# Optimization experiments

Hardware: AMD Instinct MI355X
Metric: run time of the kernel (lower is better)

The kernel has to match this reference:

```python
import jax, jax.numpy as jnp
import numpy as np

N, D, E, TOP_K = 2048, 512, 16, 2
HID = 4 * D
EPS = 1e-10


def setup_inputs() -> dict:
    key = jax.random.key(0)
    ks = jax.random.split(key, 8)
    s = 0.02
    return {
        "x": jax.random.normal(ks[0], (N, D), dtype=jnp.float32),
        "w_norm": jnp.ones((D,), dtype=jnp.float32),
        "Wr": jax.random.normal(ks[1], (D, E), dtype=jnp.float32) * s,
        "br": jnp.zeros((E,), dtype=jnp.float32),
        "W1": jax.random.normal(ks[2], (E, D, HID), dtype=jnp.float32) * s,
        "b1": jnp.zeros((E, HID), dtype=jnp.float32),
        "W2": jax.random.normal(ks[3], (E, HID, D), dtype=jnp.float32) * s,
        "b2": jnp.zeros((E, D), dtype=jnp.float32),
    }


def reference(x, w_norm, Wr, br, W1, b1, W2, b2):
    res = x
    # RMSNorm over feature dim (dim=1 in the torch code for 2D input)
    rms = jnp.sqrt(jnp.mean(x * x, axis=1, keepdims=True) + EPS)
    xn = w_norm * (x / rms)
    # Router: top-k over expert logits, softmax over the k selected logits
    logits = xn @ Wr + br                      # [N, E]
    top_p, top_i = jax.lax.top_k(logits, TOP_K)  # [N, k]
    top_p = jax.nn.softmax(top_p, axis=-1)
    # Dense per-token expert weights [N, E] (top-k indices are distinct)
    weight = jnp.zeros((x.shape[0], E), dtype=x.dtype)
    weight = weight.at[jnp.arange(x.shape[0])[:, None], top_i].add(top_p)
    # All-expert FFN (dense reference for the routed dispatch)
    h = jnp.einsum("nd,edh->enh", xn, W1) + b1[:, None, :]   # [E, N, 4D]
    y = jnp.einsum("enh,ehd->end", jax.nn.silu(h), W2) + b2[:, None, :]  # [E, N, D]
    out = jnp.einsum("end,ne->nd", y, weight)
    return out + res
```

## Files before the change

kernel.cpp:

```cpp
#include <hip/hip_runtime.h>

#define N_TOK 2048
#define DIM   512
#define NEXP  16
#define HID   2048
#define NSLOT (N_TOK*2)

typedef __attribute__((ext_vector_type(8))) short short8;
typedef __attribute__((ext_vector_type(4))) float floatx4;

__device__ __forceinline__ ushort f2bf(float f) {
    union { float f; unsigned u; } c; c.f = f;
    unsigned u = c.u;
    unsigned r = (u + 0x7fffu + ((u >> 16) & 1u)) >> 16;
    return (ushort)r;
}
__device__ __forceinline__ float bf2f(ushort u) {
    union { unsigned u; float f; } c; c.u = ((unsigned)u) << 16;
    return c.f;
}

__device__ __forceinline__ void gl_lds16(const void* g, void* l) {
    __builtin_amdgcn_global_load_lds(
        (const __attribute__((address_space(1))) unsigned int*)g,
        (__attribute__((address_space(3))) unsigned int*)l, 16, 0, 0);
}

__device__ __forceinline__ void transpose_tile(const float* __restrict__ src,
                                               ushort* __restrict__ dst,
                                               int K, int Nn, int bx, void* smem)
{
    float* Ls = (float*)smem;
    const int NT = Nn >> 6;
    const int KT = K >> 6;
    const int nt = bx % NT; bx /= NT;
    const int kt = bx % KT; bx /= KT;
    const int e  = bx;
    const int t = threadIdx.x;

    const float* sp = src + ((size_t)e * K + kt * 64) * Nn + nt * 64;
#pragma unroll
    for (int i = 0; i < 4; i++) {
        const int k  = (t >> 4) + i * 16;
        const int c4 = (t & 15) * 4;
        const float4 v = *(const float4*)(sp + (size_t)k * Nn + c4);
        Ls[k * 65 + c4 + 0] = v.x;
        Ls[k * 65 + c4 + 1] = v.y;
        Ls[k * 65 + c4 + 2] = v.z;
        Ls[k * 65 + c4 + 3] = v.w;
    }
    __syncthreads();

    ushort* dp = dst + ((size_t)e * Nn + nt * 64) * K + kt * 64;
#pragma unroll
    for (int i = 0; i < 2; i++) {
        const int n = (t >> 3) + i * 32;
        const int c = t & 7;
        unsigned w[4];
#pragma unroll
        for (int q = 0; q < 4; q++) {
            const unsigned lo = f2bf(Ls[(c * 8 + q * 2 + 0) * 65 + n]);
            const unsigned hi = f2bf(Ls[(c * 8 + q * 2 + 1) * 65 + n]);
            w[q] = lo | (hi << 16);
        }
        uint4 o = make_uint4(w[0], w[1], w[2], w[3]);
        *(uint4*)(dp + (size_t)n * K + c * 8) = o;
    }
}

__global__ __launch_bounds__(256)
void router_fused(const float* __restrict__ x, const float* __restrict__ w_norm,
                  const float* __restrict__ Wr, const float* __restrict__ br,
                  ushort* __restrict__ xn, int2* __restrict__ rec_e,
                  float2* __restrict__ rec_w)
{
    __shared__ float xs[16][516];
    __shared__ float wrT[16][516];

    const int tid  = threadIdx.x;
    const int wave = tid >> 6, lane = tid & 63;
    const int tblk = blockIdx.x * 16;

#pragma unroll
    for (int k = 0; k < 32; k++) {
        const int idx = tid + k * 256;
        wrT[idx & 15][idx >> 4] = Wr[idx];
    }

    const float4* wnp = (const float4*)w_norm;
    const float4 wa = wnp[lane], wb = wnp[lane + 64];
#pragma unroll
    for (int i = 0; i < 4; i++) {
        const int tl = wave * 4 + i, t = tblk + tl;
        const float4* xp = (const float4*)(x + (size_t)t * DIM);
        const float4 a = xp[lane], b = xp[lane + 64];
        float ss = a.x*a.x + a.y*a.y + a.z*a.z + a.w*a.w
                 + b.x*b.x + b.y*b.y + b.z*b.z + b.w*b.w;
#pragma unroll
        for (int m = 32; m >= 1; m >>= 1) ss += __shfl_xor(ss, m, 64);
        const float rinv = 1.f / sqrtf(ss * (1.f / (float)DIM) + 1e-10f);
        float4 na, nb;
        na.x = a.x * wa.x * rinv; na.y = a.y * wa.y * rinv;
        na.z = a.z * wa.z * rinv; na.w = a.w * wa.w * rinv;
        nb.x = b.x * wb.x * rinv; nb.y = b.y * wb.y * rinv;
        nb.z = b.z * wb.z * rinv; nb.w = b.w * wb.w * rinv;
        *(float4*)&xs[tl][lane * 4]       = na;
        *(float4*)&xs[tl][256 + lane * 4] = nb;
        ushort4 ua, ub;
        ua.x = f2bf(na.x); ua.y = f2bf(na.y); ua.z = f2bf(na.z); ua.w = f2bf(na.w);
        ub.x = f2bf(nb.x); ub.y = f2bf(nb.y); ub.z = f2bf(nb.z); ub.w = f2bf(nb.w);
        ushort4* xo = (ushort4*)(xn + (size_t)t * DIM);
        xo[lane] = ua; xo[lane + 64] = ub;
    }
    __syncthreads();

    const int tl = tid >> 4, e = tid & 15;
    const int t = tblk + tl;
    float acc = 0.f;
#pragma unroll 4
    for (int d = 0; d < DIM; d += 4) {
        const float4 xv = *(const float4*)&xs[tl][d];
        const float4 wv = *(const float4*)&wrT[e][d];
        acc += xv.x * wv.x + xv.y * wv.y + xv.z * wv.z + xv.w * wv.w;
    }
    const float v = acc + br[e];

    float m0 = v; int i0 = e; float m1 = -1e30f; int i1 = 16;
#pragma unroll
    for (int msk = 1; msk < 16; msk <<= 1) {
        const float om0 = __shfl_xor(m0, msk, 64); const int oi0 = __shfl_xor(i0, msk, 64);
        const float om1 = __shfl_xor(m1, msk, 64); const int oi1 = __shfl_xor(i1, msk, 64);
        const bool bf_ = (om0 > m0) || (om0 == m0 && oi0 < i0);
        const float t0m = bf_ ? om0 : m0; const int t0i = bf_ ? oi0 : i0;
        const float l0m = bf_ ? m0 : om0; const int l0i = bf_ ? i0 : oi0;
        const bool b2_ = (om1 > m1) || (om1 == m1 && oi1 < i1);
        const float t2m = b2_ ? om1 : m1; const int t2i = b2_ ? oi1 : i1;
        const bool lw = (l0m > t2m) || (l0m == t2m && l0i < t2i);
        m0 = t0m; i0 = t0i;
        m1 = lw ? l0m : t2m; i1 = lw ? l0i : t2i;
    }
    if (e == 0) {
        const float ex = expf(m1 - m0);
        const float w0 = 1.f / (1.f + ex);
        rec_e[t] = make_int2(i0, i1);
        rec_w[t] = make_float2(w0, ex * w0);
    }
}

__global__ __launch_bounds__(256)
void plan_trw1_kernel(const int2* __restrict__ rec_e, int* __restrict__ cnt,
                      int* __restrict__ off, int* __restrict__ tok_of_slot,
                      int* __restrict__ rec_slot,
                      const float* __restrict__ w1src, ushort* __restrict__ w1dst)
{
    __shared__ __align__(16) char smem[16640];

    if (blockIdx.x != 0) {
        transpose_tile(w1src, w1dst, DIM, HID, blockIdx.x - 1, smem);
        return;
    }

    int* soff = (int*)smem;
    const int tid = threadIdx.x;
    const int wv = tid >> 6, lane = tid & 63;

#pragma unroll
    for (int s = 0; s < 4; s++) {
        const int e = wv * 4 + s;
        int total = 0;
        for (int c = 0; c < N_TOK / 64; c++) {
            const int2 er = rec_e[c * 64 + lane];
            const bool hit = (er.x == e) || (er.y == e);
            total += __popcll(__ballot(hit));
        }
        if (lane == 0) soff[e + 1] = total;
    }
    __syncthreads();
    if (tid == 0) {
        soff[0] = 0;
        for (int q = 1; q <= 16; q++) soff[q] += soff[q - 1];
    }
    __syncthreads();

#pragma unroll
    for (int s = 0; s < 4; s++) {
        const int e = wv * 4 + s;
        int base = soff[e];
        if (lane == 0) { cnt[e] = soff[e + 1] - base; off[e] = base; }
        for (int c = 0; c < N_TOK / 64; c++) {
            const int t = c * 64 + lane;
            const int2 er = rec_e[t];
            const bool hit = (er.x == e) || (er.y == e);
            const unsigned long long b = __ballot(hit);
            if (hit) {
                const int slot = base + __popcll(b & ((1ull << lane) - 1ull));
                tok_of_slot[slot] = t;
                const int which = (er.y == e) ? 1 : 0;
                rec_slot[t * 2 + which] = slot;
            }
            base += __popcll(b);
        }
    }
}

template<int MODE>
__device__ __forceinline__ void gemm_body(const ushort* __restrict__ A, int a_stride,
                 const ushort* __restrict__ WT, int wt_k,
                 const float* __restrict__ bias,
                 const int* __restrict__ cnt, const int* __restrict__ off,
                 const int* __restrict__ tok_of_slot,
                 ushort* __restrict__ hout, ushort* __restrict__ yout,
                 int flat, void* smem)
{
    const int x = flat & 7;
    const int g = flat >> 3;
    int e, mt, nb, z;
    if (MODE == 0) {
        e  = x + ((g >> 7) << 3);
        const int r = g & 127;
        nb = r & 31; mt = r >> 5; z = 0;
    } else {
        const int G = ((g >> 5) << 3) + x;
        e = G >> 2; z = G & 3;
        const int idx = g & 31;
        mt = idx >> 3; nb = idx & 7;
    }

    const int count = cnt[e];
    if (mt * 128 >= count) return;
    const int base = off[e];
    const int rows = min(128, count - mt * 128);
    const int n0   = nb * 64;
    const int Nn   = (MODE == 0) ? HID : DIM;
    const int kbeg = (MODE == 0) ? 0 : (z * 512);
    ushort* yp = (MODE == 0) ? nullptr : (yout + (size_t)z * NSLOT * DIM);

    ushort* As_ = (ushort*)smem;
    ushort* Bs_ = (ushort*)((char*)smem + 16384);
    int*    toks = (int*)((char*)smem + 24576);

    const int tid = threadIdx.x;
    if (tid < 128) {
        const int r = tid < rows ? tid : rows - 1;
        const int slot = base + mt * 128 + r;
        toks[tid] = (MODE == 0) ? tok_of_slot[slot] : slot;
    }
    __syncthreads();

    const int lane = tid & 63;
    const int wid  = tid >> 6;
    const int wm = wid >> 1, wn = wid & 1;
    const int fr = lane & 15, fg = lane >> 4;

    const int rl  = lane >> 2;
    const int sko = ((lane & 3) ^ ((lane >> 4) & 3)) * 8;

    const ushort* aptr[2];
    const ushort* wbase = WT + (size_t)e * Nn * wt_k + (size_t)n0 * wt_k;
#pragma unroll
    for (int j = 0; j < 2; j++) {
        const int s = wid * 2 + j;
        aptr[j] = A + (size_t)toks[s * 16 + rl] * a_stride + sko;
    }
    const ushort* bptr = wbase + (size_t)(wid * 16 + rl) * wt_k + sko;

    floatx4 acc[4][2];
#pragma unroll
    for (int mi = 0; mi < 4; mi++)
#pragma unroll
        for (int ni = 0; ni < 2; ni++)
#pragma unroll
            for (int r = 0; r < 4; r++) acc[mi][ni][r] = 0.f;

#define STAGE(pb, k0)                                                              \
    do {                                                                           \
        _Pragma("unroll")                                                          \
        for (int j = 0; j < 2; j++)                                                \
            gl_lds16(aptr[j] + (k0), (void*)(&As_[(pb) * 4096 + (wid * 2 + j) * 512])); \
        gl_lds16(bptr + (k0), (void*)(&Bs_[(pb) * 2048 + wid * 512]));             \
    } while (0)

    int cur = 0;
    STAGE(0, kbeg);

    const int cxor = (fr >> 2) & 3;
    for (int kt = 0; kt < 16; kt++) {
        if (kt < 15) {
            STAGE(cur ^ 1, kbeg + (kt + 1) * 32);
            asm volatile("s_waitcnt vmcnt(3)" ::: "memory");
        } else {
            asm volatile("s_waitcnt vmcnt(0)" ::: "memory");
        }
        __builtin_amdgcn_s_barrier();
        __builtin_amdgcn_sched_barrier(0);

        __builtin_amdgcn_s_setprio(1);
        {
            const int co = (fg ^ cxor) * 8;
            short8 af[4], bfr[2];
#pragma unroll
            for (int mi = 0; mi < 4; mi++)
                af[mi] = *(const short8*)&As_[cur * 4096 + (wm * 64 + mi * 16 + fr) * 32 + co];
#pragma unroll
            for (int ni = 0; ni < 2; ni++)
                bfr[ni] = *(const short8*)&Bs_[cur * 2048 + (wn * 32 + ni * 16 + fr) * 32 + co];
#pragma unroll
            for (int mi = 0; mi < 4; mi++)
#pragma unroll
                for (int ni = 0; ni < 2; ni++)
                    acc[mi][ni] = __builtin_amdgcn_mfma_f32_16x16x32_bf16(af[mi], bfr[ni], acc[mi][ni], 0, 0, 0);
        }
        __builtin_amdgcn_s_setprio(0);

        __builtin_amdgcn_sched_barrier(0);
        __builtin_amdgcn_s_barrier();
        cur ^= 1;
    }
#undef STAGE

#pragma unroll
    for (int ni = 0; ni < 2; ni++) {
        const int gn = n0 + wn * 32 + ni * 16 + fr;
        const float bv = (MODE == 0) ? bias[e * HID + gn] : 0.f;
#pragma unroll
        for (int mi = 0; mi < 4; mi++) {
#pragma unroll
            for (int r = 0; r < 4; r++) {
                const int lm = wm * 64 + mi * 16 + fg * 4 + r;
                if (lm < rows) {
                    const int slot = base + mt * 128 + lm;
                    float v = acc[mi][ni][r];
                    if (MODE == 0) {
                        v += bv;
                        v = v / (1.f + __expf(-v));
                        hout[(size_t)slot * HID + gn] = f2bf(v);
                    } else {
                        yp[(size_t)slot * DIM + gn] = f2bf(v);
                    }
                }
            }
        }
    }
}

__global__ __launch_bounds__(256)
void gemm1_trw2_kernel(const ushort* __restrict__ A,
                       const ushort* __restrict__ W1T,
                       const float* __restrict__ b1,
                       const int* __restrict__ cnt, const int* __restrict__ off,
                       const int* __restrict__ tok_of_slot,
                       ushort* __restrict__ hout,
                       const float* __restrict__ w2src, ushort* __restrict__ w2dst)
{
    __shared__ __align__(16) char smem[25088];
    if (blockIdx.y >= 64) {
        const int bx = (blockIdx.y - 64) * 32 + blockIdx.x;
        transpose_tile(w2src, w2dst, HID, DIM, bx, smem);
        return;
    }
    const int flat = blockIdx.x + (blockIdx.y << 5);
    gemm_body<0>(A, DIM, W1T, DIM, b1, cnt, off, tok_of_slot, hout, nullptr,
                 flat, smem);
}

__global__ __launch_bounds__(256)
void gemm2_kernel(const ushort* __restrict__ A,
                  const ushort* __restrict__ W2T,
                  const int* __restrict__ cnt, const int* __restrict__ off,
                  ushort* __restrict__ yout)
{
    __shared__ __align__(16) char smem[25088];
    const int flat = blockIdx.x + (blockIdx.y << 5);
    gemm_body<1>(A, HID, W2T, HID, nullptr, cnt, off, nullptr, nullptr, yout,
                 flat, smem);
}

__global__ __launch_bounds__(128)
void gather_kernel(const float* __restrict__ x, const ushort* __restrict__ ypart,
                   const float* __restrict__ b2,
                   const int2* __restrict__ rec_e, const float2* __restrict__ rec_w,
                   const int2* __restrict__ rec_slot, float* __restrict__ out)
{
    const int t = blockIdx.x;
    const int d4 = threadIdx.x * 4;
    const int2 ei = rec_e[t];
    const float2 w = rec_w[t];
    const int2 sl = rec_slot[t];
    const float4 xv  = *(const float4*)(x  + (size_t)t * DIM + d4);
    float4 s0 = make_float4(0.f, 0.f, 0.f, 0.f);
    float4 s1 = make_float4(0.f, 0.f, 0.f, 0.f);
#pragma unroll
    for (int kc = 0; kc < 4; kc++) {
        const ushort* yp = ypart + (size_t)kc * NSLOT * DIM;
        const ushort4 a = *(const ushort4*)(yp + (size_t)sl.x * DIM + d4);
        const ushort4 b = *(const ushort4*)(yp + (size_t)sl.y * DIM + d4);
        s0.x += bf2f(a.x); s0.y += bf2f(a.y); s0.z += bf2f(a.z); s0.w += bf2f(a.w);
        s1.x += bf2f(b.x); s1.y += bf2f(b.y); s1.z += bf2f(b.z); s1.w += bf2f(b.w);
    }
    const float4 b0  = *(const float4*)(b2 + (size_t)ei.x * DIM + d4);
    const float4 b1v = *(const float4*)(b2 + (size_t)ei.y * DIM + d4);
    float4 o;
    o.x = xv.x + w.x * (s0.x + b0.x) + w.y * (s1.x + b1v.x);
    o.y = xv.y + w.x * (s0.y + b0.y) + w.y * (s1.y + b1v.y);
    o.z = xv.z + w.x * (s0.z + b0.z) + w.y * (s1.z + b1v.z);
    o.w = xv.w + w.x * (s0.w + b0.w) + w.y * (s1.w + b1v.w);
    *(float4*)(out + (size_t)t * DIM + d4) = o;
}

extern "C" void kernel_launch(void* const* d_in, const int* in_sizes, int n_in,
                              void* d_out, int out_size, void* d_ws, size_t ws_size,
                              hipStream_t stream)
{
    const float* x  = (const float*)d_in[0];
    const float* wn = (const float*)d_in[1];
    const float* Wr = (const float*)d_in[2];
    const float* br = (const float*)d_in[3];
    const float* W1 = (const float*)d_in[4];
    const float* b1 = (const float*)d_in[5];
    const float* W2 = (const float*)d_in[6];
    const float* b2 = (const float*)d_in[7];
    float* out = (float*)d_out;

    char* ws = (char*)d_ws;
    ushort* W1T   = (ushort*)(ws);
    ushort* W2T   = (ushort*)(ws + (32u << 20));
    ushort* xn    = (ushort*)(ws + (64u << 20));
    ushort* h_buf = (ushort*)(ws + (66u << 20));
    ushort* y_par = (ushort*)(ws + (82u << 20));
    char* p = ws + (114u << 20);
    int*    cnt         = (int*)p;    p += 256;
    int*    off         = (int*)p;    p += 256;
    int2*   rec_e       = (int2*)p;   p += N_TOK * 8;
    float2* rec_w       = (float2*)p; p += N_TOK * 8;
    int2*   rec_slot    = (int2*)p;   p += N_TOK * 8;
    int*    tok_of_slot = (int*)p;    p += NSLOT * 4;

    router_fused<<<N_TOK / 16, 256, 0, stream>>>(x, wn, Wr, br, xn, rec_e, rec_w);

    plan_trw1_kernel<<<1 + NEXP * 8 * 32, 256, 0, stream>>>(
        rec_e, cnt, off, tok_of_slot, (int*)rec_slot, W1, W1T);

    gemm1_trw2_kernel<<<dim3(32, 192), 256, 0, stream>>>(
        xn, W1T, b1, cnt, off, tok_of_slot, h_buf, W2, W2T);

    gemm2_kernel<<<dim3(32, 64), 256, 0, stream>>>(h_buf, W2T, cnt, off, y_par);

    gather_kernel<<<N_TOK, 128, 0, stream>>>(x, y_par, b2, rec_e, rec_w, rec_slot, out);
}
```

Before: 116.2 us.

## Remove split-K from second expert GEMM and write fp32 output directly

```diff
diff --git a/kernel.cpp b/kernel.cpp
--- a/kernel.cpp
+++ b/kernel.cpp
@@ -209,21 +209,20 @@
                  const float* __restrict__ bias,
                  const int* __restrict__ cnt, const int* __restrict__ off,
                  const int* __restrict__ tok_of_slot,
-                 ushort* __restrict__ hout, ushort* __restrict__ yout,
+                 ushort* __restrict__ hout, float* __restrict__ yout,
                  int flat, void* smem)
 {
     const int x = flat & 7;
     const int g = flat >> 3;
-    int e, mt, nb, z;
+    int e, mt, nb;
     if (MODE == 0) {
         e  = x + ((g >> 7) << 3);
         const int r = g & 127;
-        nb = r & 31; mt = r >> 5; z = 0;
+        nb = r & 31; mt = r >> 5;
     } else {
-        const int G = ((g >> 5) << 3) + x;
-        e = G >> 2; z = G & 3;
-        const int idx = g & 31;
-        mt = idx >> 3; nb = idx & 7;
+        e  = x + ((g >> 5) << 3);
+        const int r = g & 31;
+        nb = r & 7; mt = r >> 3;
     }
 
     const int count = cnt[e];
@@ -232,8 +231,7 @@
     const int rows = min(128, count - mt * 128);
     const int n0   = nb * 64;
     const int Nn   = (MODE == 0) ? HID : DIM;
-    const int kbeg = (MODE == 0) ? 0 : (z * 512);
-    ushort* yp = (MODE == 0) ? nullptr : (yout + (size_t)z * NSLOT * DIM);
+    const int NKT  = (MODE == 0) ? 16 : 64;
 
     ushort* As_ = (ushort*)smem;
     ushort* Bs_ = (ushort*)((char*)smem + 16384);
@@ -281,12 +279,12 @@
     } while (0)
 
     int cur = 0;
-    STAGE(0, kbeg);
+    STAGE(0, 0);
 
     const int cxor = (fr >> 2) & 3;
-    for (int kt = 0; kt < 16; kt++) {
-        if (kt < 15) {
-            STAGE(cur ^ 1, kbeg + (kt + 1) * 32);
+    for (int kt = 0; kt < NKT; kt++) {
+        if (kt < NKT - 1) {
+            STAGE(cur ^ 1, (kt + 1) * 32);
             asm volatile("s_waitcnt vmcnt(3)" ::: "memory");
         } else {
             asm volatile("s_waitcnt vmcnt(0)" ::: "memory");
@@ -335,7 +333,7 @@
                         v = v / (1.f + __expf(-v));
                         hout[(size_t)slot * HID + gn] = f2bf(v);
                     } else {
-                        yp[(size_t)slot * DIM + gn] = f2bf(v);
+                        yout[(size_t)slot * DIM + gn] = v;
                     }
                 }
             }
@@ -367,7 +365,7 @@
 void gemm2_kernel(const ushort* __restrict__ A,
                   const ushort* __restrict__ W2T,
                   const int* __restrict__ cnt, const int* __restrict__ off,
-                  ushort* __restrict__ yout)
+                  float* __restrict__ yout)
 {
     __shared__ __align__(16) char smem[25088];
     const int flat = blockIdx.x + (blockIdx.y << 5);
@@ -376,7 +374,7 @@
 }
 
 __global__ __launch_bounds__(128)
-void gather_kernel(const float* __restrict__ x, const ushort* __restrict__ ypart,
+void gather_kernel(const float* __restrict__ x, const float* __restrict__ y,
                    const float* __restrict__ b2,
                    const int2* __restrict__ rec_e, const float2* __restrict__ rec_w,
                    const int2* __restrict__ rec_slot, float* __restrict__ out)
@@ -386,17 +384,9 @@
     const int2 ei = rec_e[t];
     const float2 w = rec_w[t];
     const int2 sl = rec_slot[t];
-    const float4 xv  = *(const float4*)(x  + (size_t)t * DIM + d4);
-    float4 s0 = make_float4(0.f, 0.f, 0.f, 0.f);
-    float4 s1 = make_float4(0.f, 0.f, 0.f, 0.f);
-#pragma unroll
-    for (int kc = 0; kc < 4; kc++) {
-        const ushort* yp = ypart + (size_t)kc * NSLOT * DIM;
-        const ushort4 a = *(const ushort4*)(yp + (size_t)sl.x * DIM + d4);
-        const ushort4 b = *(const ushort4*)(yp + (size_t)sl.y * DIM + d4);
-        s0.x += bf2f(a.x); s0.y += bf2f(a.y); s0.z += bf2f(a.z); s0.w += bf2f(a.w);
-        s1.x += bf2f(b.x); s1.y += bf2f(b.y); s1.z += bf2f(b.z); s1.w += bf2f(b.w);
-    }
+    const float4 xv = *(const float4*)(x + (size_t)t * DIM + d4);
+    const float4 s0 = *(const float4*)(y + (size_t)sl.x * DIM + d4);
+    const float4 s1 = *(const float4*)(y + (size_t)sl.y * DIM + d4);
     const float4 b0  = *(const float4*)(b2 + (size_t)ei.x * DIM + d4);
     const float4 b1v = *(const float4*)(b2 + (size_t)ei.y * DIM + d4);
     float4 o;
@@ -426,7 +416,7 @@
     ushort* W2T   = (ushort*)(ws + (32u << 20));
     ushort* xn    = (ushort*)(ws + (64u << 20));
     ushort* h_buf = (ushort*)(ws + (66u << 20));
-    ushort* y_par = (ushort*)(ws + (82u << 20));
+    float*  y_buf = (float*) (ws + (82u << 20));
     char* p = ws + (114u << 20);
     int*    cnt         = (int*)p;    p += 256;
     int*    off         = (int*)p;    p += 256;
@@ -443,7 +433,7 @@
     gemm1_trw2_kernel<<<dim3(32, 192), 256, 0, stream>>>(
         xn, W1T, b1, cnt, off, tok_of_slot, h_buf, W2, W2T);
 
-    gemm2_kernel<<<dim3(32, 64), 256, 0, stream>>>(h_buf, W2T, cnt, off, y_par);
-
-    gather_kernel<<<N_TOK, 128, 0, stream>>>(x, y_par, b2, rec_e, rec_w, rec_slot, out);
-}
+    gemm2_kernel<<<dim3(32, 16), 256, 0, stream>>>(h_buf, W2T, cnt, off, y_buf);
+
+    gather_kernel<<<N_TOK, 128, 0, stream>>>(x, y_buf, b2, rec_e, rec_w, rec_slot, out);
+}
```

Result: slower. 120.2 us (+3.4%).
